# Kernel optimization log

Hardware: AMD Instinct MI355X
Metric: run time of the kernel (lower is better)

The kernel has to match this reference:

```python
import jax, jax.numpy as jnp
import numpy as np
from jax import lax

WIN = 7
K1, K2 = 0.01, 0.03
NP_ = WIN * WIN
COV_NORM = NP_ / (NP_ - 1)


def _box_filter(t, w):
    # t: [B, C, H, W] -> valid 7x7 box mean, [B, C, H-6, W-6]
    B, C, H, W = t.shape
    o = lax.conv_general_dilated(
        t.reshape(B * C, 1, H, W), w, window_strides=(1, 1), padding='VALID',
        dimension_numbers=('NCHW', 'OIHW', 'NCHW'))
    return o.reshape(B, C, H - WIN + 1, W - WIN + 1)


def setup_inputs() -> dict:
    key = jax.random.key(0)
    kx, ky = jax.random.split(key)
    X = jax.random.uniform(kx, (32, 3, 512, 512), dtype=jnp.float32)
    Y = jax.random.uniform(ky, (32, 3, 512, 512), dtype=jnp.float32)
    return {"X": X, "Y": Y}


def reference(X, Y):
    data_range = 1.0
    C1 = (K1 * data_range) ** 2
    C2 = (K2 * data_range) ** 2
    w = jnp.full((1, 1, WIN, WIN), 1.0 / NP_, dtype=X.dtype)

    ux = _box_filter(X, w)
    uy = _box_filter(Y, w)
    uxx = _box_filter(X * X, w)
    uyy = _box_filter(Y * Y, w)
    uxy = _box_filter(X * Y, w)

    vx = COV_NORM * (uxx - ux * ux)
    vy = COV_NORM * (uyy - uy * uy)
    vxy = COV_NORM * (uxy - ux * uy)

    A1 = 2 * ux * uy + C1
    A2 = 2 * vxy + C2
    B1 = ux * ux + uy * uy + C1
    B2 = vx + vy + C2
    S = (A1 * A2) / (B1 * B2)
    # reduced=True: per-channel means then mean over channels == global mean
    # (all channels have identical spatial size)
    return 1.0 - jnp.mean(S)
```

## Files before the change

kernel.cpp:

```cpp
#include <hip/hip_runtime.h>


#define IW    512
#define OUTW  506
#define BAND  6
#define NBANDS 85
#define NIMG  96
#define WPB   4
#define NBLK  (NBANDS * NIMG / WPB)
#define NPART NBLK
#define C1N2  0.2401f
#define C2N2  2.1609f
#define KA    (49.0f/24.0f)
#define KB    (49.0f/48.0f)
#define TOTAL_OUT 24579456.0f

__device__ __forceinline__ float ssim_raw(float Sx, float Sy, float S2, float Sxy) {
    float sxsy = Sx * Sy;
    float p    = fmaf(Sx, Sx, Sy * Sy);
    float a1   = fmaf(2.0f, sxsy, C1N2);
    float b1   = p + C1N2;
    float a2   = fmaf(KA, fmaf(49.0f, Sxy, -sxsy), C2N2);
    float b2   = fmaf(KB, fmaf(49.0f, S2, -p), C2N2);
    return (a1 * a2) * __builtin_amdgcn_rcpf(b1 * b2);
}

__device__ __forceinline__ void unpack8(float4 a, float4 b, float* d) {
    d[0]=a.x; d[1]=a.y; d[2]=a.z; d[3]=a.w;
    d[4]=b.x; d[5]=b.y; d[6]=b.z; d[7]=b.w;
}

__global__ __launch_bounds__(256)
void ssim_main(const float* __restrict__ X,
               const float* __restrict__ Y,
               float* __restrict__ partials) {
    __shared__ float wsum[WPB];
    const int t    = threadIdx.x;
    const int wv   = t >> 6;
    const int lane = t & 63;
    const int gw   = blockIdx.x * WPB + wv;
    const int img  = gw / NBANDS;
    const int band = gw - img * NBANDS;
    const int r0   = band * BAND;
    const float4* X4 = (const float4*)X + (size_t)img * (IW * IW / 4);
    const float4* Y4 = (const float4*)Y + (size_t)img * (IW * IW / 4);
    const int c0 = 2 * lane;

    float sx[8], sy[8], s2[8], sxy[8];
#pragma unroll
    for (int q = 0; q < 8; ++q) { sx[q]=0.f; sy[q]=0.f; s2[q]=0.f; sxy[q]=0.f; }

#pragma unroll
    for (int i = 0; i < 6; ++i) {
        const int ro = (r0 + i) * (IW / 4);
        float4 xa = X4[ro + c0], xb = X4[ro + c0 + 1];
        float4 ya = Y4[ro + c0], yb = Y4[ro + c0 + 1];
        float x[8], y[8];
        unpack8(xa, xb, x); unpack8(ya, yb, y);
#pragma unroll
        for (int q = 0; q < 8; ++q) {
            sx[q] += x[q]; sy[q] += y[q];
            s2[q]  = fmaf(x[q], x[q], s2[q]);
            s2[q]  = fmaf(y[q], y[q], s2[q]);
            sxy[q] = fmaf(x[q], y[q], sxy[q]);
        }
    }

    float accS = 0.0f;

#pragma unroll 1
    for (int r = 0; r < BAND; ++r) {
        const int orow = r0 + r;
        if (orow >= OUTW) break;

        {
            const int rn = (orow + 6) * (IW / 4);
            float4 xa = X4[rn + c0], xb = X4[rn + c0 + 1];
            float4 ya = Y4[rn + c0], yb = Y4[rn + c0 + 1];
            float x[8], y[8];
            unpack8(xa, xb, x); unpack8(ya, yb, y);
#pragma unroll
            for (int q = 0; q < 8; ++q) {
                sx[q] += x[q]; sy[q] += y[q];
                s2[q]  = fmaf(x[q], x[q], s2[q]);
                s2[q]  = fmaf(y[q], y[q], s2[q]);
                sxy[q] = fmaf(x[q], y[q], sxy[q]);
            }
        }

        float Wx[8], Wy[8], W2[8], Wxy[8];
#define HWIN(S, W)                                                         \
        {                                                                  \
            float h0 = __shfl_down(S[0], 1, 64);                           \
            float h1 = __shfl_down(S[1], 1, 64);                           \
            float h2 = __shfl_down(S[2], 1, 64);                           \
            float h3 = __shfl_down(S[3], 1, 64);                           \
            float h4 = __shfl_down(S[4], 1, 64);                           \
            float h5 = __shfl_down(S[5], 1, 64);                           \
            W[0] = ((S[0]+S[1]) + (S[2]+S[3])) + ((S[4]+S[5]) + S[6]);     \
            W[1] = W[0] + (S[7] - S[0]);                                   \
            W[2] = W[1] + (h0   - S[1]);                                   \
            W[3] = W[2] + (h1   - S[2]);                                   \
            W[4] = W[3] + (h2   - S[3]);                                   \
            W[5] = W[4] + (h3   - S[4]);                                   \
            W[6] = W[5] + (h4   - S[5]);                                   \
            W[7] = W[6] + (h5   - S[6]);                                   \
        }
        HWIN(sx,  Wx)
        HWIN(sy,  Wy)
        HWIN(s2,  W2)
        HWIN(sxy, Wxy)
#undef HWIN

#pragma unroll
        for (int m = 0; m < 8; ++m) {
            float Sv = ssim_raw(Wx[m], Wy[m], W2[m], Wxy[m]);
            accS += (8 * lane + m < OUTW) ? Sv : 0.0f;
        }

        {
            const int rr = orow * (IW / 4);
            float4 xa = X4[rr + c0], xb = X4[rr + c0 + 1];
            float4 ya = Y4[rr + c0], yb = Y4[rr + c0 + 1];
            float x[8], y[8];
            unpack8(xa, xb, x); unpack8(ya, yb, y);
#pragma unroll
            for (int q = 0; q < 8; ++q) {
                sx[q] -= x[q]; sy[q] -= y[q];
                s2[q]  = fmaf(-x[q], x[q], s2[q]);
                s2[q]  = fmaf(-y[q], y[q], s2[q]);
                sxy[q] = fmaf(-x[q], y[q], sxy[q]);
            }
        }
    }

#pragma unroll
    for (int o = 32; o > 0; o >>= 1)
        accS += __shfl_down(accS, o, 64);
    if (lane == 0) wsum[wv] = accS;
    __syncthreads();
    if (t == 0)
        partials[blockIdx.x] = (wsum[0] + wsum[1]) + (wsum[2] + wsum[3]);
}

__global__ __launch_bounds__(256) void ssim_finalize(const float* __restrict__ partials,
                                                     float* __restrict__ out) {
    __shared__ float wsum[4];
    const int t = threadIdx.x;
    float v = 0.0f;
    for (int i = t; i < NPART; i += 256) v += partials[i];
#pragma unroll
    for (int o = 32; o > 0; o >>= 1)
        v += __shfl_down(v, o, 64);
    if ((t & 63) == 0) wsum[t >> 6] = v;
    __syncthreads();
    if (t == 0)
        out[0] = 1.0f - ((wsum[0] + wsum[1]) + (wsum[2] + wsum[3])) / TOTAL_OUT;
}

extern "C" void kernel_launch(void* const* d_in, const int* in_sizes, int n_in,
                              void* d_out, int out_size, void* d_ws, size_t ws_size,
                              hipStream_t stream) {
    const float* X = (const float*)d_in[0];
    const float* Y = (const float*)d_in[1];
    float* partials = (float*)d_ws;
    float* out = (float*)d_out;

    hipLaunchKernelGGL(ssim_main, dim3(NBLK), dim3(256), 0, stream,
                       X, Y, partials);
    hipLaunchKernelGGL(ssim_finalize, dim3(1), dim3(256), 0, stream,
                       partials, out);
}
```

Before: 241.4 us.

## Prefetch incoming rows into per-wave LDS ring via global_load_lds

Each wave now loads the incoming rows of X and Y asynchronously into a double-buffered LDS ring with global_load_lds, staying two rows ahead of the sliding window. Each iteration then reads the new row from LDS instead of issuing direct global loads. The aim is to hide global-memory latency in a kernel that appears latency-bound. The cost is 32KB of LDS per block, which may limit occupancy, and a coarse vmcnt(0) wait each iteration. There is also no explicit ordering between the LDS reads and the next global_load_lds that overwrites the same buffer.

```diff
diff --git a/kernel.cpp b/kernel.cpp
--- a/kernel.cpp
+++ b/kernel.cpp
@@ -15,6 +15,14 @@
 #define KB    (49.0f/48.0f)
 #define TOTAL_OUT 24579456.0f
 
+typedef const __attribute__((address_space(1))) unsigned int* gas1_t;
+typedef __attribute__((address_space(3))) unsigned int* las3_t;
+
+__device__ __forceinline__ void stage_row(const float* g, float* l, int lane) {
+    __builtin_amdgcn_global_load_lds((gas1_t)(g + 4 * lane),       (las3_t)l,         16, 0, 0);
+    __builtin_amdgcn_global_load_lds((gas1_t)(g + 256 + 4 * lane), (las3_t)(l + 256), 16, 0, 0);
+}
+
 __device__ __forceinline__ float ssim_raw(float Sx, float Sy, float S2, float Sxy) {
     float sxsy = Sx * Sy;
     float p    = fmaf(Sx, Sx, Sy * Sy);
@@ -34,7 +42,8 @@
 void ssim_main(const float* __restrict__ X,
                const float* __restrict__ Y,
                float* __restrict__ partials) {
-    __shared__ float wsum[WPB];
+    __shared__ float ring[WPB][2][1024];
+
     const int t    = threadIdx.x;
     const int wv   = t >> 6;
     const int lane = t & 63;
@@ -42,9 +51,16 @@
     const int img  = gw / NBANDS;
     const int band = gw - img * NBANDS;
     const int r0   = band * BAND;
-    const float4* X4 = (const float4*)X + (size_t)img * (IW * IW / 4);
-    const float4* Y4 = (const float4*)Y + (size_t)img * (IW * IW / 4);
+    const float* Xf = X + (size_t)img * IW * IW;
+    const float* Yf = Y + (size_t)img * IW * IW;
+    const float4* X4 = (const float4*)Xf;
+    const float4* Y4 = (const float4*)Yf;
     const int c0 = 2 * lane;
+
+    stage_row(Xf + (size_t)(r0 + 6) * IW, &ring[wv][0][0],   lane);
+    stage_row(Yf + (size_t)(r0 + 6) * IW, &ring[wv][0][512], lane);
+    stage_row(Xf + (size_t)(r0 + 7) * IW, &ring[wv][1][0],   lane);
+    stage_row(Yf + (size_t)(r0 + 7) * IW, &ring[wv][1][512], lane);
 
     float sx[8], sy[8], s2[8], sxy[8];
 #pragma unroll
@@ -72,11 +88,15 @@
     for (int r = 0; r < BAND; ++r) {
         const int orow = r0 + r;
         if (orow >= OUTW) break;
-
+        const int p = r & 1;
+
+        asm volatile("s_waitcnt vmcnt(0)" ::: "memory");
         {
-            const int rn = (orow + 6) * (IW / 4);
-            float4 xa = X4[rn + c0], xb = X4[rn + c0 + 1];
-            float4 ya = Y4[rn + c0], yb = Y4[rn + c0 + 1];
+            const float* sl = &ring[wv][p][0];
+            float4 xa = *(const float4*)(sl + 8 * lane);
+            float4 xb = *(const float4*)(sl + 8 * lane + 4);
+            float4 ya = *(const float4*)(sl + 512 + 8 * lane);
+            float4 yb = *(const float4*)(sl + 512 + 8 * lane + 4);
             float x[8], y[8];
             unpack8(xa, xb, x); unpack8(ya, yb, y);
 #pragma unroll
@@ -86,6 +106,11 @@
                 s2[q]  = fmaf(y[q], y[q], s2[q]);
                 sxy[q] = fmaf(x[q], y[q], sxy[q]);
             }
+        }
+
+        if (r + 2 < BAND && orow + 2 < OUTW) {
+            stage_row(Xf + (size_t)(orow + 8) * IW, &ring[wv][p][0],   lane);
+            stage_row(Yf + (size_t)(orow + 8) * IW, &ring[wv][p][512], lane);
         }
 
         float Wx[8], Wy[8], W2[8], Wxy[8];
@@ -137,6 +162,8 @@
 #pragma unroll
     for (int o = 32; o > 0; o >>= 1)
         accS += __shfl_down(accS, o, 64);
+    __syncthreads();
+    float* wsum = &ring[0][0][0];
     if (lane == 0) wsum[wv] = accS;
     __syncthreads();
     if (t == 0)
```

Measured after the change: 235.0 us. 2.6% less time.
